# Performance work log

Hardware: AMD Instinct MI355X
Metric: run time of the kernel (lower is better)

Reference implementation:

```python
import jax, jax.numpy as jnp
import numpy as np

N = 50000
E = 800000
DIN = 128
DH = [128, 128]
DOUT = 64


def setup_inputs() -> dict:
    key = jax.random.key(0)
    ks = jax.random.split(key, 12)

    def w(k, fan_in, fan_out):
        return jax.random.normal(k, (fan_in, fan_out), dtype=jnp.float32) / np.sqrt(fan_in)

    x = jax.random.normal(ks[0], (N, DIN), dtype=jnp.float32)
    edge_index = jax.random.randint(ks[1], (2, E), 0, N, dtype=jnp.int64)
    return {
        "x": x,
        "edge_index": edge_index,
        # SAGEConv layer 0: lin_l (aggregated neighbors, with bias), lin_r (root, no bias)
        "Wl0": w(ks[2], DIN, DH[0]), "Wr0": w(ks[3], DIN, DH[0]), "b0": jnp.zeros((DH[0],), jnp.float32),
        # SAGEConv layer 1
        "Wl1": w(ks[4], DH[0], DH[1]), "Wr1": w(ks[5], DH[0], DH[1]), "b1": jnp.zeros((DH[1],), jnp.float32),
        # final Linear
        "Wout": w(ks[6], DH[1], DOUT), "bout": jnp.zeros((DOUT,), jnp.float32),
    }


def sage_conv(h, src, dst, Wl, Wr, b):
    # mean-aggregate source features at destination nodes
    msg = h[src]                                                  # [E, d]
    agg = jax.ops.segment_sum(msg, dst, num_segments=N)           # [N, d]
    cnt = jax.ops.segment_sum(jnp.ones((src.shape[0],), h.dtype), dst, num_segments=N)
    agg = agg / jnp.maximum(cnt, 1.0)[:, None]
    return agg @ Wl + h @ Wr + b


def reference(x, edge_index, Wl0, Wr0, b0, Wl1, Wr1, b1, Wout, bout):
    src, dst = edge_index[0], edge_index[1]
    h = jax.nn.relu(sage_conv(x, src, dst, Wl0, Wr0, b0))
    # dropout: identity in eval mode
    h = jax.nn.relu(sage_conv(h, src, dst, Wl1, Wr1, b1))
    out = h @ Wout + bout                                         # [N, DOUT]
    return jax.nn.softmax(out, axis=1)
```

## Files before the change

### kernel.cpp

```cpp
#include <hip/hip_runtime.h>


#define CAP 64
#define NBK 256
#define EPB 2048
#define BCAP8 768
#define ASTR 136

typedef __attribute__((ext_vector_type(8))) short bf16x8;
typedef __attribute__((ext_vector_type(4))) float f32x4;

__device__ __forceinline__ unsigned short bf16_rtne(float f) {
    unsigned u = __float_as_uint(f);
    u += 0x7FFFu + ((u >> 16) & 1u);
    return (unsigned short)(u >> 16);
}

__device__ __forceinline__ unsigned pack2(float lo, float hi) {
    return (unsigned)bf16_rtne(lo) | ((unsigned)bf16_rtne(hi) << 16);
}

__device__ __forceinline__ void pack_w_body(const float* __restrict__ Wl,
                                            const float* __restrict__ Wr,
                                            unsigned short* __restrict__ Wp, int i) {
    int j = i & 7;
    int l = (i >> 3) & 63;
    int ntile = (i >> 9) & 7;
    int kstep = i >> 12;
    int k = kstep * 32 + (l >> 4) * 8 + j;
    int n = ntile * 16 + (l & 15);
    float v = (k < 128) ? Wl[k * 128 + n] : Wr[(k - 128) * 128 + n];
    Wp[i] = bf16_rtne(v);
}

__global__ __launch_bounds__(256) void bucket_prep_kernel(
        const int* __restrict__ src, const int* __restrict__ dst,
        unsigned int* __restrict__ gtail, unsigned int* __restrict__ gbuf,
        int E, int aBlocks,
        const float* __restrict__ x, unsigned short* __restrict__ xb, int n4, int cvtBlocks,
        const float* __restrict__ Wl0, const float* __restrict__ Wr0,
        unsigned short* __restrict__ Wp1,
        const float* __restrict__ Wl1, const float* __restrict__ Wr1,
        unsigned short* __restrict__ Wp2,
        const float* __restrict__ Wout, unsigned short* __restrict__ Wpo) {
    int b = blockIdx.x;
    if (b < aBlocks) {
        __shared__ unsigned int hist[NBK];
        __shared__ unsigned int pref[NBK + 1];
        __shared__ int baseS[NBK];
        __shared__ unsigned int scat[EPB];
        __shared__ unsigned char scatb[EPB];
        int tid = (int)threadIdx.x;
        int xcd = b & 7;
        hist[tid] = 0u;
        __syncthreads();

        int e0 = b * EPB + tid * 8;
        int dd[8], ss[8], bb[8];
        unsigned rr[8];
        bool vld[8];
        if (e0 + 7 < E) {
            int4 d0 = *(const int4*)(dst + e0);
            int4 d1 = *(const int4*)(dst + e0 + 4);
            int4 s0 = *(const int4*)(src + e0);
            int4 s1 = *(const int4*)(src + e0 + 4);
            dd[0] = d0.x; dd[1] = d0.y; dd[2] = d0.z; dd[3] = d0.w;
            dd[4] = d1.x; dd[5] = d1.y; dd[6] = d1.z; dd[7] = d1.w;
            ss[0] = s0.x; ss[1] = s0.y; ss[2] = s0.z; ss[3] = s0.w;
            ss[4] = s1.x; ss[5] = s1.y; ss[6] = s1.z; ss[7] = s1.w;
#pragma unroll
            for (int u = 0; u < 8; ++u) vld[u] = true;
        } else {
#pragma unroll
            for (int u = 0; u < 8; ++u) {
                int e = e0 + u;
                vld[u] = (e < E);
                dd[u] = vld[u] ? dst[e] : 0;
                ss[u] = vld[u] ? src[e] : 0;
            }
        }
#pragma unroll
        for (int u = 0; u < 8; ++u) {
            bb[u] = dd[u] >> 8;
            rr[u] = vld[u] ? atomicAdd(&hist[bb[u]], 1u) : 0u;
        }
        __syncthreads();
        pref[tid + 1] = hist[tid];
        if (tid == 0) pref[0] = 0u;
        __syncthreads();
        for (int off = 1; off < NBK; off <<= 1) {
            unsigned add = (tid + 1 > off) ? pref[tid + 1 - off] : 0u;
            __syncthreads();
            pref[tid + 1] += add;
            __syncthreads();
        }
        {
            unsigned h = hist[tid];
            unsigned gb0 = (h != 0u) ? atomicAdd(&gtail[xcd * NBK + tid], h) : 0u;
            baseS[tid] = (int)((unsigned)(xcd * NBK + tid) * BCAP8 + gb0) - (int)pref[tid];
        }
        __syncthreads();
#pragma unroll
        for (int u = 0; u < 8; ++u) {
            if (vld[u]) {
                unsigned idx = pref[bb[u]] + rr[u];
                scat[idx] = ((unsigned)dd[u] << 16) | (unsigned)(ss[u] & 0xFFFF);
                scatb[idx] = (unsigned char)bb[u];
            }
        }
        __syncthreads();
        unsigned tot = pref[NBK];
        for (unsigned i = (unsigned)tid; i < tot; i += 256u) {
            int bk = (int)scatb[i];
            int gi = baseS[bk] + (int)i;
            unsigned segBase = (unsigned)(xcd * NBK + bk) * BCAP8;
            if ((unsigned)gi - segBase < BCAP8) gbuf[gi] = scat[i];
        }
    } else if (b < aBlocks + cvtBlocks) {
        int i = (b - aBlocks) * 256 + (int)threadIdx.x;
        if (i < n4) {
            float4 v = ((const float4*)x)[i];
            ushort4 o;
            o.x = bf16_rtne(v.x); o.y = bf16_rtne(v.y);
            o.z = bf16_rtne(v.z); o.w = bf16_rtne(v.w);
            ((ushort4*)xb)[i] = o;
        }
    } else if (b < aBlocks + cvtBlocks + 128) {
        pack_w_body(Wl0, Wr0, Wp1, (b - aBlocks - cvtBlocks) * 256 + (int)threadIdx.x);
    } else if (b < aBlocks + cvtBlocks + 256) {
        pack_w_body(Wl1, Wr1, Wp2, (b - aBlocks - cvtBlocks - 128) * 256 + (int)threadIdx.x);
    } else {
        int i = (b - aBlocks - cvtBlocks - 256) * 256 + (int)threadIdx.x;
        int j = i & 7;
        int l = (i >> 3) & 63;
        int nt = (i >> 9) & 3;
        int ks = i >> 11;
        int k = ks * 32 + (l >> 4) * 8 + j;
        int n = nt * 16 + (l & 15);
        Wpo[i] = bf16_rtne(Wout[k * 64 + n]);
    }
}

__global__ __launch_bounds__(256) void fill_csr_kernel(
        const unsigned int* __restrict__ gtail, const unsigned int* __restrict__ gbuf,
        int* __restrict__ cnt, unsigned short* __restrict__ csr, int N) {
    __shared__ unsigned int cntL[256];
    __shared__ unsigned short stage[256 * CAP];
    int b = blockIdx.x;
    int tid = (int)threadIdx.x;
    cntL[tid] = 0u;
    __syncthreads();
#pragma unroll 1
    for (int xcd = 0; xcd < 8; ++xcd) {
        unsigned nE = gtail[xcd * NBK + b];
        if (nE > BCAP8) nE = BCAP8;
        const unsigned int* g = gbuf + (size_t)(xcd * NBK + b) * BCAP8;
        for (unsigned i = (unsigned)tid; i < nE; i += 256u) {
            unsigned pk = g[i];
            int dl = (int)((pk >> 16) & 255u);
            unsigned p = atomicAdd(&cntL[dl], 1u);
            if (p < CAP) stage[dl * CAP + p] = (unsigned short)(pk & 0xFFFFu);
        }
    }
    __syncthreads();
    const uint4* s4 = (const uint4*)stage;
    uint4* g4 = (uint4*)(csr + (size_t)b * (256 * CAP));
    for (int i = tid; i < (256 * CAP) / 8; i += 256) g4[i] = s4[i];
    int node = b * 256 + tid;
    if (node < N) cnt[node] = (int)cntL[tid];
}

__device__ __forceinline__ void gather_mean_lds(
        const unsigned short* __restrict__ hb, const int* __restrict__ cnt,
        const unsigned short* __restrict__ csr, unsigned short* __restrict__ sAw,
        int m0, int lane, int N) {
    int qw = lane >> 4;
    int ql = lane & 15;
    const uint4* h4 = (const uint4*)hb;
#pragma unroll 1
    for (int i = 0; i < 4; ++i) {
        int nl = qw * 4 + i;
        int node = m0 + nl;
        int deg = (node < N) ? min(cnt[node], CAP) : 0;
        int s0 = node * CAP;
        int s1 = s0 + deg;
        float a[8];
#pragma unroll
        for (int u = 0; u < 8; ++u) a[u] = 0.f;
        for (int base = 0; base < deg; base += 16) {
            int nc = min(16, deg - base);
            int e = min(s0 + base + ql, s1 - 1);
            int idx = csr[e];
            for (int j = 0; j < nc; j += 8) {
                uint4 v[8];
#pragma unroll
                for (int u = 0; u < 8; ++u) {
                    int sidx = __shfl(idx, j + u, 16);
                    v[u] = h4[(size_t)sidx * 16 + ql];
                }
#pragma unroll
                for (int u = 0; u < 8; ++u) {
                    bool ok = (j + u < nc);
                    unsigned w0 = ok ? v[u].x : 0u;
                    unsigned w1 = ok ? v[u].y : 0u;
                    unsigned w2 = ok ? v[u].z : 0u;
                    unsigned w3 = ok ? v[u].w : 0u;
                    a[0] += __uint_as_float(w0 << 16);
                    a[1] += __uint_as_float(w0 & 0xFFFF0000u);
                    a[2] += __uint_as_float(w1 << 16);
                    a[3] += __uint_as_float(w1 & 0xFFFF0000u);
                    a[4] += __uint_as_float(w2 << 16);
                    a[5] += __uint_as_float(w2 & 0xFFFF0000u);
                    a[6] += __uint_as_float(w3 << 16);
                    a[7] += __uint_as_float(w3 & 0xFFFF0000u);
                }
            }
        }
        float inv = 1.0f / (float)max(deg, 1);
        uint4 o;
        o.x = pack2(a[0] * inv, a[1] * inv);
        o.y = pack2(a[2] * inv, a[3] * inv);
        o.z = pack2(a[4] * inv, a[5] * inv);
        o.w = pack2(a[6] * inv, a[7] * inv);
        *(uint4*)(sAw + nl * ASTR + ql * 8) = o;
    }
}

__device__ __forceinline__ void mfma_dual_gemm_lds(
        const unsigned short* __restrict__ sAw, const unsigned short* __restrict__ rootb,
        const unsigned short* __restrict__ Wp, int rowc, int quad, int c, int lane,
        f32x4 acc[8]) {
#pragma unroll
    for (int t = 0; t < 8; ++t) acc[t] = (f32x4){0.f, 0.f, 0.f, 0.f};
    for (int ks = 0; ks < 8; ++ks) {
        bf16x8 a;
        if (ks < 4) a = *(const bf16x8*)(sAw + c * ASTR + ks * 32 + quad * 8);
        else        a = *(const bf16x8*)(rootb + (size_t)rowc * 128 + (ks & 3) * 32 + quad * 8);
#pragma unroll
        for (int t = 0; t < 8; ++t) {
            bf16x8 bf = *(const bf16x8*)(Wp + ((size_t)(ks * 8 + t) * 64 + lane) * 8);
            acc[t] = __builtin_amdgcn_mfma_f32_16x16x32_bf16(a, bf, acc[t], 0, 0, 0);
        }
    }
}

__global__ __launch_bounds__(256) void fused_l1_kernel(
        const unsigned short* __restrict__ hb, const int* __restrict__ cnt,
        const unsigned short* __restrict__ csr, const unsigned short* __restrict__ Wp,
        const float* __restrict__ b, unsigned short* __restrict__ houtb, int N) {
    __shared__ unsigned short sA[4][16 * ASTR];
    int lane = threadIdx.x & 63;
    int wv = threadIdx.x >> 6;
    int m0 = blockIdx.x * 64 + wv * 16;
    gather_mean_lds(hb, cnt, csr, &sA[wv][0], m0, lane, N);
    int quad = lane >> 4;
    int c = lane & 15;
    int rowc = min(m0 + c, N - 1);
    f32x4 acc[8];
    mfma_dual_gemm_lds(&sA[wv][0], hb, Wp, rowc, quad, c, lane, acc);
#pragma unroll
    for (int t = 0; t < 8; ++t) {
        int col = t * 16 + c;
        float bias = b[col];
#pragma unroll
        for (int r = 0; r < 4; ++r) {
            int node = m0 + quad * 4 + r;
            if (node < N) {
                float v = fmaxf(acc[t][r] + bias, 0.f);
                houtb[(size_t)node * 128 + col] = bf16_rtne(v);
            }
        }
    }
}

__global__ __launch_bounds__(256) void fused_l2_kernel(
        const unsigned short* __restrict__ hb, const int* __restrict__ cnt,
        const unsigned short* __restrict__ csr, const unsigned short* __restrict__ Wp,
        const float* __restrict__ b,
        const unsigned short* __restrict__ Wpo, const float* __restrict__ bout,
        float* __restrict__ out, int N) {
    __shared__ unsigned short sA[4][16 * ASTR];
    int lane = threadIdx.x & 63;
    int wv = threadIdx.x >> 6;
    int m0 = blockIdx.x * 64 + wv * 16;
    gather_mean_lds(hb, cnt, csr, &sA[wv][0], m0, lane, N);
    int quad = lane >> 4;
    int c = lane & 15;
    int rowc = min(m0 + c, N - 1);
    f32x4 acc[8];
    mfma_dual_gemm_lds(&sA[wv][0], hb, Wp, rowc, quad, c, lane, acc);
#pragma unroll
    for (int t = 0; t < 8; ++t) {
        int col = t * 16 + c;
        float bias = b[col];
#pragma unroll
        for (int r = 0; r < 4; ++r) {
            sA[wv][(quad * 4 + r) * ASTR + col] = bf16_rtne(fmaxf(acc[t][r] + bias, 0.f));
        }
    }

    f32x4 acc2[4];
#pragma unroll
    for (int nt = 0; nt < 4; ++nt) acc2[nt] = (f32x4){0.f, 0.f, 0.f, 0.f};
#pragma unroll
    for (int ks = 0; ks < 4; ++ks) {
        bf16x8 a = *(const bf16x8*)&sA[wv][c * ASTR + ks * 32 + quad * 8];
#pragma unroll
        for (int nt = 0; nt < 4; ++nt) {
            bf16x8 bf = *(const bf16x8*)(Wpo + ((size_t)(ks * 4 + nt) * 64 + lane) * 8);
            acc2[nt] = __builtin_amdgcn_mfma_f32_16x16x32_bf16(a, bf, acc2[nt], 0, 0, 0);
        }
    }

    float bo[4];
#pragma unroll
    for (int nt = 0; nt < 4; ++nt) bo[nt] = bout[nt * 16 + c];
#pragma unroll
    for (int r = 0; r < 4; ++r) {
        float v[4];
#pragma unroll
        for (int nt = 0; nt < 4; ++nt) v[nt] = acc2[nt][r] + bo[nt];
        float m = fmaxf(fmaxf(v[0], v[1]), fmaxf(v[2], v[3]));
#pragma unroll
        for (int ofs = 1; ofs < 16; ofs <<= 1) m = fmaxf(m, __shfl_xor(m, ofs, 64));
        float e[4];
        float s = 0.f;
#pragma unroll
        for (int nt = 0; nt < 4; ++nt) { e[nt] = __expf(v[nt] - m); s += e[nt]; }
#pragma unroll
        for (int ofs = 1; ofs < 16; ofs <<= 1) s += __shfl_xor(s, ofs, 64);
        float inv = 1.0f / s;
        int node = m0 + quad * 4 + r;
        if (node < N) {
#pragma unroll
            for (int nt = 0; nt < 4; ++nt)
                out[(size_t)node * 64 + nt * 16 + c] = e[nt] * inv;
        }
    }
}

extern "C" void kernel_launch(void* const* d_in, const int* in_sizes, int n_in,
                              void* d_out, int out_size, void* d_ws, size_t ws_size,
                              hipStream_t stream) {
    const float* x    = (const float*)d_in[0];
    const int*   ei   = (const int*)d_in[1];
    const float* Wl0  = (const float*)d_in[2];
    const float* Wr0  = (const float*)d_in[3];
    const float* b0   = (const float*)d_in[4];
    const float* Wl1  = (const float*)d_in[5];
    const float* Wr1  = (const float*)d_in[6];
    const float* b1   = (const float*)d_in[7];
    const float* Wout = (const float*)d_in[8];
    const float* bout = (const float*)d_in[9];

    int N = in_sizes[0] / 128;
    int E = in_sizes[1] / 2;
    const int* src = ei;
    const int* dst = ei + E;
    int nb = (N + 255) >> 8;

    char* p = (char*)d_ws;
    auto alloc = [&](size_t bytes) -> char* {
        char* r = p;
        p += (bytes + 255) & ~(size_t)255;
        return r;
    };
    unsigned int*   gtail = (unsigned int*)alloc((size_t)8 * NBK * 4);
    unsigned int*   gbuf  = (unsigned int*)alloc((size_t)8 * NBK * BCAP8 * 4);
    int*            cnt   = (int*)alloc((size_t)N * 4);
    unsigned short* csr   = (unsigned short*)alloc((size_t)nb * 256 * CAP * 2);
    unsigned short* xb    = (unsigned short*)alloc((size_t)N * 128 * 2);
    unsigned short* h0b   = (unsigned short*)alloc((size_t)N * 128 * 2);
    unsigned short* Wp1   = (unsigned short*)alloc((size_t)32768 * 2);
    unsigned short* Wp2   = (unsigned short*)alloc((size_t)32768 * 2);
    unsigned short* Wpo   = (unsigned short*)alloc((size_t)8192 * 2);

    hipMemsetAsync(gtail, 0, (size_t)8 * NBK * 4, stream);

    int n4 = N * 128 / 4;
    int cvtBlocks = (n4 + 255) / 256;
    int aBlocks = (E + EPB - 1) / EPB;
    bucket_prep_kernel<<<aBlocks + cvtBlocks + 256 + 32, 256, 0, stream>>>(
        src, dst, gtail, gbuf, E, aBlocks,
        x, xb, n4, cvtBlocks, Wl0, Wr0, Wp1, Wl1, Wr1, Wp2, Wout, Wpo);

    fill_csr_kernel<<<nb, 256, 0, stream>>>(gtail, gbuf, cnt, csr, N);

    int gb = (N + 63) / 64;
    fused_l1_kernel<<<gb, 256, 0, stream>>>(xb, cnt, csr, Wp1, b0, h0b, N);
    fused_l2_kernel<<<gb, 256, 0, stream>>>(h0b, cnt, csr, Wp2, b1,
                                            Wpo, bout, (float*)d_out, N);
}
```

Before: 186.6 us.

## Split neighbor gather into four column slices and stage layer-1 output through LDS

The gather-mean loop now walks the 128-wide feature row in four 32-column slices. Each lane loads one 32-bit word per neighbor instead of a 16-byte vector, which cuts live registers (two accumulators instead of eight) and may raise occupancy. The cost is that every neighbor index is re-read and re-shuffled four times, with four times as many narrower global loads. Separately, the layer-1 epilogue writes the bf16 outputs to LDS first, then stores full 16-byte rows to global memory instead of scattered 2-byte stores.

```diff
diff --git a/kernel.cpp b/kernel.cpp
--- a/kernel.cpp
+++ b/kernel.cpp
@@ -171,58 +171,50 @@
 }
 
 __device__ __forceinline__ void gather_mean_lds(
-        const unsigned short* __restrict__ hb, const int* __restrict__ cnt,
+        const unsigned* __restrict__ hu,
+        const int* __restrict__ cnt,
         const unsigned short* __restrict__ csr, unsigned short* __restrict__ sAw,
         int m0, int lane, int N) {
     int qw = lane >> 4;
     int ql = lane & 15;
-    const uint4* h4 = (const uint4*)hb;
+    int degs[4], bases[4];
+#pragma unroll
+    for (int i = 0; i < 4; ++i) {
+        int node = m0 + qw * 4 + i;
+        degs[i] = (node < N) ? min(cnt[node], CAP) : 0;
+        bases[i] = node * CAP;
+    }
 #pragma unroll 1
-    for (int i = 0; i < 4; ++i) {
-        int nl = qw * 4 + i;
-        int node = m0 + nl;
-        int deg = (node < N) ? min(cnt[node], CAP) : 0;
-        int s0 = node * CAP;
-        int s1 = s0 + deg;
-        float a[8];
-#pragma unroll
-        for (int u = 0; u < 8; ++u) a[u] = 0.f;
-        for (int base = 0; base < deg; base += 16) {
-            int nc = min(16, deg - base);
-            int e = min(s0 + base + ql, s1 - 1);
-            int idx = csr[e];
-            for (int j = 0; j < nc; j += 8) {
-                uint4 v[8];
-#pragma unroll
-                for (int u = 0; u < 8; ++u) {
-                    int sidx = __shfl(idx, j + u, 16);
-                    v[u] = h4[(size_t)sidx * 16 + ql];
-                }
-#pragma unroll
-                for (int u = 0; u < 8; ++u) {
-                    bool ok = (j + u < nc);
-                    unsigned w0 = ok ? v[u].x : 0u;
-                    unsigned w1 = ok ? v[u].y : 0u;
-                    unsigned w2 = ok ? v[u].z : 0u;
-                    unsigned w3 = ok ? v[u].w : 0u;
-                    a[0] += __uint_as_float(w0 << 16);
-                    a[1] += __uint_as_float(w0 & 0xFFFF0000u);
-                    a[2] += __uint_as_float(w1 << 16);
-                    a[3] += __uint_as_float(w1 & 0xFFFF0000u);
-                    a[4] += __uint_as_float(w2 << 16);
-                    a[5] += __uint_as_float(w2 & 0xFFFF0000u);
-                    a[6] += __uint_as_float(w3 << 16);
-                    a[7] += __uint_as_float(w3 & 0xFFFF0000u);
+    for (int s = 0; s < 4; ++s) {
+#pragma unroll 1
+        for (int i = 0; i < 4; ++i) {
+            int nl = qw * 4 + i;
+            int deg = degs[i];
+            int s0 = bases[i];
+            int s1 = s0 + deg;
+            float a0 = 0.f, a1 = 0.f;
+            for (int base = 0; base < deg; base += 16) {
+                int nc = min(16, deg - base);
+                int e = min(s0 + base + ql, s1 - 1);
+                int idx = csr[e];
+                for (int j = 0; j < nc; j += 8) {
+                    unsigned v[8];
+#pragma unroll
+                    for (int u = 0; u < 8; ++u) {
+                        int sidx = __shfl(idx, j + u, 16);
+                        v[u] = hu[(size_t)sidx * 64 + s * 16 + ql];
+                    }
+#pragma unroll
+                    for (int u = 0; u < 8; ++u) {
+                        unsigned w = (j + u < nc) ? v[u] : 0u;
+                        a0 += __uint_as_float(w << 16);
+                        a1 += __uint_as_float(w & 0xFFFF0000u);
+                    }
                 }
             }
-        }
-        float inv = 1.0f / (float)max(deg, 1);
-        uint4 o;
-        o.x = pack2(a[0] * inv, a[1] * inv);
-        o.y = pack2(a[2] * inv, a[3] * inv);
-        o.z = pack2(a[4] * inv, a[5] * inv);
-        o.w = pack2(a[6] * inv, a[7] * inv);
-        *(uint4*)(sAw + nl * ASTR + ql * 8) = o;
+            float inv = 1.0f / (float)max(deg, 1);
+            *(unsigned*)(sAw + nl * ASTR + s * 32 + ql * 2) = pack2(a0 * inv, a1 * inv);
+        }
     }
 }
 
@@ -252,7 +244,7 @@
     int lane = threadIdx.x & 63;
     int wv = threadIdx.x >> 6;
     int m0 = blockIdx.x * 64 + wv * 16;
-    gather_mean_lds(hb, cnt, csr, &sA[wv][0], m0, lane, N);
+    gather_mean_lds((const unsigned*)hb, cnt, csr, &sA[wv][0], m0, lane, N);
     int quad = lane >> 4;
     int c = lane & 15;
     int rowc = min(m0 + c, N - 1);
@@ -264,10 +256,18 @@
         float bias = b[col];
 #pragma unroll
         for (int r = 0; r < 4; ++r) {
-            int node = m0 + quad * 4 + r;
+            sA[wv][(quad * 4 + r) * ASTR + col] = bf16_rtne(fmaxf(acc[t][r] + bias, 0.f));
+        }
+    }
+    {
+        int qw = lane >> 4, ql = lane & 15;
+#pragma unroll
+        for (int i = 0; i < 4; ++i) {
+            int nl = qw * 4 + i;
+            int node = m0 + nl;
             if (node < N) {
-                float v = fmaxf(acc[t][r] + bias, 0.f);
-                houtb[(size_t)node * 128 + col] = bf16_rtne(v);
+                uint4 row = *(const uint4*)(&sA[wv][nl * ASTR + ql * 8]);
+                *(uint4*)(houtb + (size_t)node * 128 + ql * 8) = row;
             }
         }
     }
@@ -283,7 +283,7 @@
     int lane = threadIdx.x & 63;
     int wv = threadIdx.x >> 6;
     int m0 = blockIdx.x * 64 + wv * 16;
-    gather_mean_lds(hb, cnt, csr, &sA[wv][0], m0, lane, N);
+    gather_mean_lds((const unsigned*)hb, cnt, csr, &sA[wv][0], m0, lane, N);
     int quad = lane >> 4;
     int c = lane & 15;
     int rowc = min(m0 + c, N - 1);
```

New measurement: 225.6 us. 20.9% more time.

## Sort CSR neighbors by source range and vectorize layer-1 output stores via LDS

Applied to the files above, without the earlier changes.

The CSR fill kernel now runs two passes: it counts edges per destination and per source-index range, prefix-sums those counts, then scatters neighbors so each node's list is grouped by source range. This is meant to give the later gathers better locality in the hidden-feature array. The layer-1 epilogue now writes bf16 results into LDS and stores each row with 16-byte vector writes instead of scattered 2-byte stores. The cost is a second pass over the edge buffer and extra LDS atomics in the fill kernel.

```diff
diff --git a/kernel.cpp b/kernel.cpp
--- a/kernel.cpp
+++ b/kernel.cpp
@@ -6,6 +6,8 @@
 #define EPB 2048
 #define BCAP8 768
 #define ASTR 136
+#define NR 4
+#define RSH 14
 
 typedef __attribute__((ext_vector_type(8))) short bf16x8;
 typedef __attribute__((ext_vector_type(4))) float f32x4;
@@ -144,11 +146,13 @@
 __global__ __launch_bounds__(256) void fill_csr_kernel(
         const unsigned int* __restrict__ gtail, const unsigned int* __restrict__ gbuf,
         int* __restrict__ cnt, unsigned short* __restrict__ csr, int N) {
-    __shared__ unsigned int cntL[256];
+    __shared__ unsigned int cntR[256 * NR];
+    __shared__ unsigned int offR[256 * NR];
     __shared__ unsigned short stage[256 * CAP];
     int b = blockIdx.x;
     int tid = (int)threadIdx.x;
-    cntL[tid] = 0u;
+#pragma unroll
+    for (int r = 0; r < NR; ++r) cntR[r * 256 + tid] = 0u;
     __syncthreads();
 #pragma unroll 1
     for (int xcd = 0; xcd < 8; ++xcd) {
@@ -158,7 +162,34 @@
         for (unsigned i = (unsigned)tid; i < nE; i += 256u) {
             unsigned pk = g[i];
             int dl = (int)((pk >> 16) & 255u);
-            unsigned p = atomicAdd(&cntL[dl], 1u);
+            int rg = (int)((pk & 0xFFFFu) >> RSH);
+            atomicAdd(&cntR[dl * NR + rg], 1u);
+        }
+    }
+    __syncthreads();
+    {
+        unsigned c0 = cntR[tid * NR + 0], c1 = cntR[tid * NR + 1];
+        unsigned c2 = cntR[tid * NR + 2], c3 = cntR[tid * NR + 3];
+        offR[tid * NR + 0] = 0u;
+        offR[tid * NR + 1] = c0;
+        offR[tid * NR + 2] = c0 + c1;
+        offR[tid * NR + 3] = c0 + c1 + c2;
+        int node = b * 256 + tid;
+        if (node < N) cnt[node] = min((int)(c0 + c1 + c2 + c3), CAP);
+        cntR[tid * NR + 0] = 0u; cntR[tid * NR + 1] = 0u;
+        cntR[tid * NR + 2] = 0u; cntR[tid * NR + 3] = 0u;
+    }
+    __syncthreads();
+#pragma unroll 1
+    for (int xcd = 0; xcd < 8; ++xcd) {
+        unsigned nE = gtail[xcd * NBK + b];
+        if (nE > BCAP8) nE = BCAP8;
+        const unsigned int* g = gbuf + (size_t)(xcd * NBK + b) * BCAP8;
+        for (unsigned i = (unsigned)tid; i < nE; i += 256u) {
+            unsigned pk = g[i];
+            int dl = (int)((pk >> 16) & 255u);
+            int rg = (int)((pk & 0xFFFFu) >> RSH);
+            unsigned p = atomicAdd(&cntR[dl * NR + rg], 1u) + offR[dl * NR + rg];
             if (p < CAP) stage[dl * CAP + p] = (unsigned short)(pk & 0xFFFFu);
         }
     }
@@ -166,17 +197,15 @@
     const uint4* s4 = (const uint4*)stage;
     uint4* g4 = (uint4*)(csr + (size_t)b * (256 * CAP));
     for (int i = tid; i < (256 * CAP) / 8; i += 256) g4[i] = s4[i];
-    int node = b * 256 + tid;
-    if (node < N) cnt[node] = (int)cntL[tid];
 }
 
 __device__ __forceinline__ void gather_mean_lds(
-        const unsigned short* __restrict__ hb, const int* __restrict__ cnt,
+        const uint4* __restrict__ h4,
+        const int* __restrict__ cnt,
         const unsigned short* __restrict__ csr, unsigned short* __restrict__ sAw,
         int m0, int lane, int N) {
     int qw = lane >> 4;
     int ql = lane & 15;
-    const uint4* h4 = (const uint4*)hb;
 #pragma unroll 1
     for (int i = 0; i < 4; ++i) {
         int nl = qw * 4 + i;
@@ -252,7 +281,7 @@
     int lane = threadIdx.x & 63;
     int wv = threadIdx.x >> 6;
     int m0 = blockIdx.x * 64 + wv * 16;
-    gather_mean_lds(hb, cnt, csr, &sA[wv][0], m0, lane, N);
+    gather_mean_lds((const uint4*)hb, cnt, csr, &sA[wv][0], m0, lane, N);
     int quad = lane >> 4;
     int c = lane & 15;
     int rowc = min(m0 + c, N - 1);
@@ -264,10 +293,18 @@
         float bias = b[col];
 #pragma unroll
         for (int r = 0; r < 4; ++r) {
-            int node = m0 + quad * 4 + r;
+            sA[wv][(quad * 4 + r) * ASTR + col] = bf16_rtne(fmaxf(acc[t][r] + bias, 0.f));
+        }
+    }
+    {
+        int qw = lane >> 4, ql = lane & 15;
+#pragma unroll
+        for (int i = 0; i < 4; ++i) {
+            int nl = qw * 4 + i;
+            int node = m0 + nl;
             if (node < N) {
-                float v = fmaxf(acc[t][r] + bias, 0.f);
-                houtb[(size_t)node * 128 + col] = bf16_rtne(v);
+                uint4 row = *(const uint4*)(&sA[wv][nl * ASTR + ql * 8]);
+                *(uint4*)(houtb + (size_t)node * 128 + ql * 8) = row;
             }
         }
     }
@@ -283,7 +320,7 @@
     int lane = threadIdx.x & 63;
     int wv = threadIdx.x >> 6;
     int m0 = blockIdx.x * 64 + wv * 16;
-    gather_mean_lds(hb, cnt, csr, &sA[wv][0], m0, lane, N);
+    gather_mean_lds((const uint4*)hb, cnt, csr, &sA[wv][0], m0, lane, N);
     int quad = lane >> 4;
     int c = lane & 15;
     int rowc = min(m0 + c, N - 1);
```

After: 187.0 us. No clear change (+0.3%).

## Replace global atomic bucket scatter with per-block sorted slabs and prefix tables

Applied to the files above, without the earlier changes.

The bucket prep kernel now writes each block's locally bucket-sorted edges as a contiguous slab, plus a packed start/end prefix table per bucket. This removes the global tail atomics, the memset and the scattered global writes. The CSR fill kernel then reads each block's range for its bucket, with one thread per source block walking a short range serially. The layer-1 output is also staged through LDS and written as 16-byte row vectors instead of scattered 2-byte stores. The trade-off is that fill_csr now does uncoalesced, serial per-thread reads across roughly 391 slabs.

```diff
diff --git a/kernel.cpp b/kernel.cpp
--- a/kernel.cpp
+++ b/kernel.cpp
@@ -4,7 +4,6 @@
 #define CAP 64
 #define NBK 256
 #define EPB 2048
-#define BCAP8 768
 #define ASTR 136
 
 typedef __attribute__((ext_vector_type(8))) short bf16x8;
@@ -35,7 +34,7 @@
 
 __global__ __launch_bounds__(256) void bucket_prep_kernel(
         const int* __restrict__ src, const int* __restrict__ dst,
-        unsigned int* __restrict__ gtail, unsigned int* __restrict__ gbuf,
+        unsigned int* __restrict__ pref2, unsigned int* __restrict__ gbuf,
         int E, int aBlocks,
         const float* __restrict__ x, unsigned short* __restrict__ xb, int n4, int cvtBlocks,
         const float* __restrict__ Wl0, const float* __restrict__ Wr0,
@@ -47,11 +46,8 @@
     if (b < aBlocks) {
         __shared__ unsigned int hist[NBK];
         __shared__ unsigned int pref[NBK + 1];
-        __shared__ int baseS[NBK];
         __shared__ unsigned int scat[EPB];
-        __shared__ unsigned char scatb[EPB];
         int tid = (int)threadIdx.x;
-        int xcd = b & 7;
         hist[tid] = 0u;
         __syncthreads();
 
@@ -94,28 +90,20 @@
             pref[tid + 1] += add;
             __syncthreads();
         }
-        {
-            unsigned h = hist[tid];
-            unsigned gb0 = (h != 0u) ? atomicAdd(&gtail[xcd * NBK + tid], h) : 0u;
-            baseS[tid] = (int)((unsigned)(xcd * NBK + tid) * BCAP8 + gb0) - (int)pref[tid];
-        }
-        __syncthreads();
 #pragma unroll
         for (int u = 0; u < 8; ++u) {
             if (vld[u]) {
                 unsigned idx = pref[bb[u]] + rr[u];
                 scat[idx] = ((unsigned)dd[u] << 16) | (unsigned)(ss[u] & 0xFFFF);
-                scatb[idx] = (unsigned char)bb[u];
             }
         }
         __syncthreads();
-        unsigned tot = pref[NBK];
-        for (unsigned i = (unsigned)tid; i < tot; i += 256u) {
-            int bk = (int)scatb[i];
-            int gi = baseS[bk] + (int)i;
-            unsigned segBase = (unsigned)(xcd * NBK + bk) * BCAP8;
-            if ((unsigned)gi - segBase < BCAP8) gbuf[gi] = scat[i];
-        }
+        {
+            uint4* g4 = (uint4*)(gbuf + (size_t)b * EPB);
+            const uint4* s4 = (const uint4*)scat;
+            for (int i = tid; i < EPB / 4; i += 256) g4[i] = s4[i];
+        }
+        pref2[(size_t)b * NBK + tid] = (pref[tid] & 0xFFFFu) | (pref[tid + 1] << 16);
     } else if (b < aBlocks + cvtBlocks) {
         int i = (b - aBlocks) * 256 + (int)threadIdx.x;
         if (i < n4) {
@@ -142,21 +130,21 @@
 }
 
 __global__ __launch_bounds__(256) void fill_csr_kernel(
-        const unsigned int* __restrict__ gtail, const unsigned int* __restrict__ gbuf,
-        int* __restrict__ cnt, unsigned short* __restrict__ csr, int N) {
+        const unsigned int* __restrict__ pref2, const unsigned int* __restrict__ gbuf,
+        int* __restrict__ cnt, unsigned short* __restrict__ csr, int N, int aBlocks) {
     __shared__ unsigned int cntL[256];
     __shared__ unsigned short stage[256 * CAP];
-    int b = blockIdx.x;
+    int bk = blockIdx.x;
     int tid = (int)threadIdx.x;
     cntL[tid] = 0u;
     __syncthreads();
-#pragma unroll 1
-    for (int xcd = 0; xcd < 8; ++xcd) {
-        unsigned nE = gtail[xcd * NBK + b];
-        if (nE > BCAP8) nE = BCAP8;
-        const unsigned int* g = gbuf + (size_t)(xcd * NBK + b) * BCAP8;
-        for (unsigned i = (unsigned)tid; i < nE; i += 256u) {
-            unsigned pk = g[i];
+    for (int b = tid; b < aBlocks; b += 256) {
+        unsigned pr = pref2[(size_t)b * NBK + bk];
+        unsigned st = pr & 0xFFFFu;
+        unsigned en = pr >> 16;
+        const unsigned int* slab = gbuf + (size_t)b * EPB;
+        for (unsigned i = st; i < en; ++i) {
+            unsigned pk = slab[i];
             int dl = (int)((pk >> 16) & 255u);
             unsigned p = atomicAdd(&cntL[dl], 1u);
             if (p < CAP) stage[dl * CAP + p] = (unsigned short)(pk & 0xFFFFu);
@@ -164,19 +152,19 @@
     }
     __syncthreads();
     const uint4* s4 = (const uint4*)stage;
-    uint4* g4 = (uint4*)(csr + (size_t)b * (256 * CAP));
+    uint4* g4 = (uint4*)(csr + (size_t)bk * (256 * CAP));
     for (int i = tid; i < (256 * CAP) / 8; i += 256) g4[i] = s4[i];
-    int node = b * 256 + tid;
-    if (node < N) cnt[node] = (int)cntL[tid];
+    int node = bk * 256 + tid;
+    if (node < N) cnt[node] = min((int)cntL[tid], CAP);
 }
 
 __device__ __forceinline__ void gather_mean_lds(
-        const unsigned short* __restrict__ hb, const int* __restrict__ cnt,
+        const uint4* __restrict__ h4,
+        const int* __restrict__ cnt,
         const unsigned short* __restrict__ csr, unsigned short* __restrict__ sAw,
         int m0, int lane, int N) {
     int qw = lane >> 4;
     int ql = lane & 15;
-    const uint4* h4 = (const uint4*)hb;
 #pragma unroll 1
     for (int i = 0; i < 4; ++i) {
         int nl = qw * 4 + i;
@@ -252,7 +240,7 @@
     int lane = threadIdx.x & 63;
     int wv = threadIdx.x >> 6;
     int m0 = blockIdx.x * 64 + wv * 16;
-    gather_mean_lds(hb, cnt, csr, &sA[wv][0], m0, lane, N);
+    gather_mean_lds((const uint4*)hb, cnt, csr, &sA[wv][0], m0, lane, N);
     int quad = lane >> 4;
     int c = lane & 15;
     int rowc = min(m0 + c, N - 1);
@@ -264,10 +252,18 @@
         float bias = b[col];
 #pragma unroll
         for (int r = 0; r < 4; ++r) {
-            int node = m0 + quad * 4 + r;
+            sA[wv][(quad * 4 + r) * ASTR + col] = bf16_rtne(fmaxf(acc[t][r] + bias, 0.f));
+        }
+    }
+    {
+        int qw = lane >> 4, ql = lane & 15;
+#pragma unroll
+        for (int i = 0; i < 4; ++i) {
+            int nl = qw * 4 + i;
+            int node = m0 + nl;
             if (node < N) {
-                float v = fmaxf(acc[t][r] + bias, 0.f);
-                houtb[(size_t)node * 128 + col] = bf16_rtne(v);
+                uint4 row = *(const uint4*)(&sA[wv][nl * ASTR + ql * 8]);
+                *(uint4*)(houtb + (size_t)node * 128 + ql * 8) = row;
             }
         }
     }
@@ -283,7 +279,7 @@
     int lane = threadIdx.x & 63;
     int wv = threadIdx.x >> 6;
     int m0 = blockIdx.x * 64 + wv * 16;
-    gather_mean_lds(hb, cnt, csr, &sA[wv][0], m0, lane, N);
+    gather_mean_lds((const uint4*)hb, cnt, csr, &sA[wv][0], m0, lane, N);
     int quad = lane >> 4;
     int c = lane & 15;
     int rowc = min(m0 + c, N - 1);
@@ -358,6 +354,7 @@
     const int* src = ei;
     const int* dst = ei + E;
     int nb = (N + 255) >> 8;
+    int aBlocks = (E + EPB - 1) / EPB;
 
     char* p = (char*)d_ws;
     auto alloc = [&](size_t bytes) -> char* {
@@ -365,8 +362,8 @@
         p += (bytes + 255) & ~(size_t)255;
         return r;
     };
-    unsigned int*   gtail = (unsigned int*)alloc((size_t)8 * NBK * 4);
-    unsigned int*   gbuf  = (unsigned int*)alloc((size_t)8 * NBK * BCAP8 * 4);
+    unsigned int*   pref2 = (unsigned int*)alloc((size_t)aBlocks * NBK * 4);
+    unsigned int*   gbuf  = (unsigned int*)alloc((size_t)aBlocks * EPB * 4);
     int*            cnt   = (int*)alloc((size_t)N * 4);
     unsigned short* csr   = (unsigned short*)alloc((size_t)nb * 256 * CAP * 2);
     unsigned short* xb    = (unsigned short*)alloc((size_t)N * 128 * 2);
@@ -375,16 +372,13 @@
     unsigned short* Wp2   = (unsigned short*)alloc((size_t)32768 * 2);
     unsigned short* Wpo   = (unsigned short*)alloc((size_t)8192 * 2);
 
-    hipMemsetAsync(gtail, 0, (size_t)8 * NBK * 4, stream);
-
     int n4 = N * 128 / 4;
     int cvtBlocks = (n4 + 255) / 256;
-    int aBlocks = (E + EPB - 1) / EPB;
     bucket_prep_kernel<<<aBlocks + cvtBlocks + 256 + 32, 256, 0, stream>>>(
-        src, dst, gtail, gbuf, E, aBlocks,
+        src, dst, pref2, gbuf, E, aBlocks,
         x, xb, n4, cvtBlocks, Wl0, Wr0, Wp1, Wl1, Wr1, Wp2, Wout, Wpo);
 
-    fill_csr_kernel<<<nb, 256, 0, stream>>>(gtail, gbuf, cnt, csr, N);
+    fill_csr_kernel<<<nb, 256, 0, stream>>>(pref2, gbuf, cnt, csr, N, aBlocks);
 
     int gb = (N + 63) / 64;
     fused_l1_kernel<<<gb, 256, 0, stream>>>(xb, cnt, csr, Wp1, b0, h0b, N);
```

Measured after the change: 187.1 us. No clear change (+0.3%).
